# Kernel tuning notes

Hardware: AMD Instinct MI355X
Metric: run time of the kernel (lower is better)

## Reference

```python
import jax, jax.numpy as jnp
import numpy as np

LN_EPS = 1e-5
SM_EPS = 1e-16  # torch_geometric softmax denominator eps


def _layernorm(x, g, b):
    mu = jnp.mean(x, axis=-1, keepdims=True)
    var = jnp.var(x, axis=-1, keepdims=True)
    return (x - mu) * jax.lax.rsqrt(var + LN_EPS) * g + b


def setup_inputs() -> dict:
    d = 128
    L = 3
    N = 50000
    E = 800000
    key = jax.random.key(0)
    ks = jax.random.split(key, 16)
    s = 1.0 / np.sqrt(d)
    inp = {
        "edge_index": jax.random.randint(ks[0], (2, E), 0, N, dtype=jnp.int32),
        "x": jax.random.normal(ks[1], (N, d), dtype=jnp.float32),
        # per-layer attention params, stacked over layers
        "Wq": jax.random.uniform(ks[2], (L, d, d), jnp.float32, -s, s),
        "bq": jax.random.uniform(ks[3], (L, d), jnp.float32, -s, s),
        "Wk": jax.random.uniform(ks[4], (L, d, d), jnp.float32, -s, s),
        "bk": jax.random.uniform(ks[5], (L, d), jnp.float32, -s, s),
        "Wv": jax.random.uniform(ks[6], (L, d, d), jnp.float32, -s, s),
        "bv": jax.random.uniform(ks[7], (L, d), jnp.float32, -s, s),
        "ln_g": jnp.ones((L, d), jnp.float32),
        "ln_b": jnp.zeros((L, d), jnp.float32),
        # MLP stack: d -> 4d -> 2d -> d (no activations, per source)
        "W1": jax.random.uniform(ks[8], (4 * d, d), jnp.float32, -s, s),
        "b1": jax.random.uniform(ks[9], (4 * d,), jnp.float32, -s, s),
        "W2": jax.random.uniform(ks[10], (2 * d, 4 * d), jnp.float32, -0.5 * s, 0.5 * s),
        "b2": jax.random.uniform(ks[11], (2 * d,), jnp.float32, -0.5 * s, 0.5 * s),
        "W3": jax.random.uniform(ks[12], (d, 2 * d), jnp.float32, -0.7 * s, 0.7 * s),
        "b3": jax.random.uniform(ks[13], (d,), jnp.float32, -0.7 * s, 0.7 * s),
        "Wvec": jax.random.uniform(ks[14], (1, d), jnp.float32, -s, s),
        "bvec": jax.random.uniform(ks[15], (1,), jnp.float32, -s, s),
        "fn_g": jnp.ones((d,), jnp.float32),
        "fn_b": jnp.zeros((d,), jnp.float32),
    }
    return inp


def reference(edge_index, x, Wq, bq, Wk, bk, Wv, bv, ln_g, ln_b,
              W1, b1, W2, b2, W3, b3, Wvec, bvec, fn_g, fn_b):
    N = x.shape[0]
    src = edge_index[0]
    dst = edge_index[1]
    x_i = x[src]  # [E, d]
    x_j = x[dst]  # [E, d]
    L = Wq.shape[0]
    attn_output = None
    query = None
    for i in range(L):
        q = x_i @ Wq[i].T + bq[i]
        k = x_j @ Wk[i].T + bk[i]
        v = x_j @ Wv[i].T + bv[i]
        alpha = jnp.sum(q * k, axis=-1)  # [E]
        # segment softmax over destination node (torch_geometric.utils.softmax)
        m = jax.ops.segment_max(alpha, dst, num_segments=N)
        e = jnp.exp(alpha - m[dst])
        s = jax.ops.segment_sum(e, dst, num_segments=N)
        alpha = e / (s[dst] + SM_EPS)
        attn_output = jax.nn.relu(alpha[:, None] * v)  # dropout = identity (eval)
        query = _layernorm(x_j + attn_output, ln_g[i], ln_b[i])
    adj = attn_output  # squeeze(0) is a no-op for [E, d]
    adj = adj @ W1.T + b1
    adj = adj @ W2.T + b2
    adj = adj @ W3.T + b3
    adj = _layernorm(adj + query, fn_g, fn_b)
    adj_logits = (adj @ Wvec.T + bvec)[:, 0]  # [E]
    return adj_logits
```

## Files before the change

### kernel.cpp

```cpp
#include <hip/hip_runtime.h>


typedef __attribute__((ext_vector_type(8))) short bf16x8;
typedef __attribute__((ext_vector_type(4))) float f32x4;

__device__ __forceinline__ unsigned short f2bf(float f) {
  unsigned int u = __float_as_uint(f);
  unsigned int r = (u + 0x7fffu + ((u >> 16) & 1u)) >> 16;
  return (unsigned short)r;
}
__device__ __forceinline__ float blo(unsigned int u) {
  return __uint_as_float(u << 16);
}
__device__ __forceinline__ float bhi(unsigned int u) {
  return __uint_as_float(u & 0xffff0000u);
}

__global__ __launch_bounds__(128) void k_TW(
    const float* __restrict__ W2, const float* __restrict__ W1,
    const float* __restrict__ Wq, const float* __restrict__ Wk,
    const float* __restrict__ Wv, float* __restrict__ T,
    unsigned short* __restrict__ Wqb, unsigned short* __restrict__ Wkb,
    unsigned short* __restrict__ Wvb, float* __restrict__ sArr, int N) {
  const int b = blockIdx.x, t = threadIdx.x;
  if (b < 256) {
    float acc = 0.f;
    for (int k = 0; k < 512; ++k) acc += W2[b * 512 + k] * W1[k * 128 + t];
    T[b * 128 + t] = acc;
  } else if (b < 640) {
    const int idx = (b - 256) * 128 + t;
    const int m = idx >> 14, i = idx & 16383;
    const float* s = (m == 0) ? Wq : (m == 1) ? Wk : Wv;
    unsigned short* d = (m == 0) ? Wqb : (m == 1) ? Wkb : Wvb;
    d[i] = f2bf(s[i]);
  } else {
    const int i = (b - 640) * 128 + t;
    if (i < N) sArr[i] = 0.f;
  }
}

__global__ __launch_bounds__(256) void k_Ac(
    const float* __restrict__ W3, const float* __restrict__ T,
    const float* __restrict__ W2, const float* __restrict__ b1,
    const float* __restrict__ b2, const float* __restrict__ b3,
    const float* __restrict__ g, const float* __restrict__ lb,
    const float* __restrict__ fg, const float* __restrict__ fb,
    const float* __restrict__ wv, unsigned short* __restrict__ A3b,
    float* __restrict__ cfull, float* __restrict__ C) {
  __shared__ float t1[256];
  __shared__ float cf[128];
  const int b = blockIdx.x, t = threadIdx.x;
  if (b < 64) {
    const int i = 2 * b + (t >> 7), j = t & 127;
    float acc = 0.f;
    for (int k = 0; k < 256; ++k) acc += W3[i * 256 + k] * T[k * 128 + j];
    A3b[i * 128 + j] = f2bf(acc);
    return;
  }
  float acc = b2[t];
  for (int c = 0; c < 512; ++c) acc += W2[t * 512 + c] * b1[c];
  t1[t] = acc;
  __syncthreads();
  if (t < 128) {
    float a = b3[t];
    for (int k = 0; k < 256; ++k) a += W3[t * 256 + k] * t1[k];
    cfull[t] = a;
    cf[t] = a;
  }
  __syncthreads();
  if (t < 64) {
    const int l = t;
    const float2 gv = ((const float2*)g)[l];
    const float2 bv = ((const float2*)lb)[l];
    const float2 fgv = ((const float2*)fg)[l];
    const float2 fbv = ((const float2*)fb)[l];
    const float2 wvv = ((const float2*)wv)[l];
    const float P0 = cf[2 * l] + bv.x, P1 = cf[2 * l + 1] + bv.y;
    const float w0 = fgv.x * wvv.x, w1 = fgv.y * wvv.y;
    float s[9];
    s[0] = P0 + P1;
    s[1] = P0 * w0 + P1 * w1;
    s[2] = P0 * P0 + P1 * P1;
    s[3] = gv.x + gv.y;
    s[4] = gv.x * w0 + gv.y * w1;
    s[5] = gv.x * gv.x + gv.y * gv.y;
    s[6] = P0 * gv.x + P1 * gv.y;
    s[7] = w0 + w1;
    s[8] = fbv.x * wvv.x + fbv.y * wvv.y;
#pragma unroll
    for (int m = 32; m >= 1; m >>= 1)
#pragma unroll
      for (int i = 0; i < 9; ++i) s[i] += __shfl_xor(s[i], m, 64);
    if (l == 0)
#pragma unroll
      for (int i = 0; i < 9; ++i) C[i] = s[i];
  }
}

__global__ __launch_bounds__(256, 3) void k_node(
    const float* __restrict__ x, const unsigned short* __restrict__ Wqb,
    const unsigned short* __restrict__ Wkb,
    const unsigned short* __restrict__ Wvb,
    const unsigned short* __restrict__ A3b, const float* __restrict__ bq,
    const float* __restrict__ bk, const float* __restrict__ bv,
    const float* __restrict__ cfull, const float* __restrict__ g,
    const float* __restrict__ lb, const float* __restrict__ fg,
    const float* __restrict__ wvp, unsigned short* __restrict__ Qb,
    unsigned short* __restrict__ Kb, float* __restrict__ S, int N) {
  __shared__ unsigned short tile[64][136];
  const int t = threadIdx.x;
  const int nb = blockIdx.x * 64;
  for (int i = t; i < 64 * 32; i += 256) {
    const int j = i >> 5, c4 = i & 31;
    const int n = nb + j;
    float4 v = make_float4(0.f, 0.f, 0.f, 0.f);
    if (n < N) v = ((const float4*)x)[(size_t)n * 32 + c4];
    unsigned int lo = f2bf(v.x) | ((unsigned int)f2bf(v.y) << 16);
    unsigned int hi = f2bf(v.z) | ((unsigned int)f2bf(v.w) << 16);
    *(uint2*)&tile[j][c4 << 2] = make_uint2(lo, hi);
  }
  __syncthreads();
  const int wv16 = __builtin_amdgcn_readfirstlane(t >> 6) * 16;
  const int l = t & 63;
  const int ln = l & 15, g4 = l >> 4;
  bf16x8 af[4];
#pragma unroll
  for (int kb = 0; kb < 4; ++kb)
    af[kb] = *(const bf16x8*)&tile[wv16 + ln][kb * 32 + g4 * 8];

#pragma unroll
  for (int cb = 0; cb < 8; ++cb) {
    f32x4 acc = {0.f, 0.f, 0.f, 0.f};
#pragma unroll
    for (int kb = 0; kb < 4; ++kb) {
      const bf16x8 bfr =
          *(const bf16x8*)(Wqb + ((cb * 16 + ln) << 7) + kb * 32 + g4 * 8);
      acc = __builtin_amdgcn_mfma_f32_16x16x32_bf16(af[kb], bfr, acc, 0, 0, 0);
    }
    const int col = cb * 16 + ln;
    const float bs = bq[col];
#pragma unroll
    for (int r = 0; r < 4; ++r) tile[wv16 + g4 * 4 + r][col] = f2bf(acc[r] + bs);
  }
#pragma unroll
  for (int c = 0; c < 4; ++c) {
    const int row = wv16 + c * 4 + g4;
    const int n = nb + row;
    if (n < N)
      ((uint4*)(Qb + (size_t)n * 128))[ln] = *(const uint4*)&tile[row][ln * 8];
  }

#pragma unroll
  for (int cb = 0; cb < 8; ++cb) {
    f32x4 acc = {0.f, 0.f, 0.f, 0.f};
#pragma unroll
    for (int kb = 0; kb < 4; ++kb) {
      const bf16x8 bfr =
          *(const bf16x8*)(Wkb + ((cb * 16 + ln) << 7) + kb * 32 + g4 * 8);
      acc = __builtin_amdgcn_mfma_f32_16x16x32_bf16(af[kb], bfr, acc, 0, 0, 0);
    }
    const int col = cb * 16 + ln;
    const float bs = bk[col];
#pragma unroll
    for (int r = 0; r < 4; ++r) tile[wv16 + g4 * 4 + r][col] = f2bf(acc[r] + bs);
  }
#pragma unroll
  for (int c = 0; c < 4; ++c) {
    const int row = wv16 + c * 4 + g4;
    const int n = nb + row;
    if (n < N)
      ((uint4*)(Kb + (size_t)n * 128))[ln] = *(const uint4*)&tile[row][ln * 8];
  }

  float uf[8][4];
#pragma unroll
  for (int cb = 0; cb < 8; ++cb) {
    f32x4 acc = {0.f, 0.f, 0.f, 0.f};
#pragma unroll
    for (int kb = 0; kb < 4; ++kb) {
      const bf16x8 bfr =
          *(const bf16x8*)(Wvb + ((cb * 16 + ln) << 7) + kb * 32 + g4 * 8);
      acc = __builtin_amdgcn_mfma_f32_16x16x32_bf16(af[kb], bfr, acc, 0, 0, 0);
    }
    const int col = cb * 16 + ln;
    const float bs = bv[col];
#pragma unroll
    for (int r = 0; r < 4; ++r) {
      const float v = fmaxf(acc[r] + bs, 0.f);
      uf[cb][r] = v;
      tile[wv16 + g4 * 4 + r][col] = f2bf(v);
    }
  }

  bf16x8 af2[4];
#pragma unroll
  for (int kb = 0; kb < 4; ++kb)
    af2[kb] = *(const bf16x8*)&tile[wv16 + ln][kb * 32 + g4 * 8];
  float vmf[8][4];
#pragma unroll
  for (int cb = 0; cb < 8; ++cb) {
    f32x4 acc = {0.f, 0.f, 0.f, 0.f};
#pragma unroll
    for (int kb = 0; kb < 4; ++kb) {
      const bf16x8 bfr =
          *(const bf16x8*)(A3b + ((cb * 16 + ln) << 7) + kb * 32 + g4 * 8);
      acc = __builtin_amdgcn_mfma_f32_16x16x32_bf16(af2[kb], bfr, acc, 0, 0, 0);
    }
#pragma unroll
    for (int r = 0; r < 4; ++r) vmf[cb][r] = acc[r];
  }

  float gc[8], wc[8], Pc[8];
#pragma unroll
  for (int cb = 0; cb < 8; ++cb) {
    const int col = cb * 16 + ln;
    gc[cb] = g[col];
    wc[cb] = fg[col] * wvp[col];
    Pc[cb] = cfull[col] + lb[col];
  }

#pragma unroll
  for (int r = 0; r < 4; ++r) {
    const int row = wv16 + g4 * 4 + r;
    const int nrow = (nb + row < N) ? (nb + row) : (N - 1);
    float s[23];
#pragma unroll
    for (int i = 0; i < 23; ++i) s[i] = 0.f;
#pragma unroll
    for (int cb = 0; cb < 8; ++cb) {
      const float xv = x[(size_t)nrow * 128 + cb * 16 + ln];
      const float u = uf[cb][r];
      const float v = vmf[cb][r];
      const float gg = gc[cb], ww = wc[cb], PP = Pc[cb];
      const float xg = xv * gg, ug = u * gg;
      s[0] += xv;
      s[1] += u;
      s[2] += xv * xv;
      s[3] += xv * u;
      s[4] += u * u;
      s[5] += v;
      s[6] += v * ww;
      s[7] += xg;
      s[8] += ug;
      s[9] += xg * ww;
      s[10] += ug * ww;
      s[11] += PP * v;
      s[12] += v * v;
      s[13] += PP * xg;
      s[14] += PP * ug;
      s[15] += v * xg;
      s[16] += v * ug;
      s[17] += v * gg;
      s[18] += xg * xg;
      s[19] += xg * ug;
      s[20] += ug * ug;
      s[21] += xg * gg;
      s[22] += ug * gg;
    }
#pragma unroll
    for (int m = 1; m <= 8; m <<= 1)
#pragma unroll
      for (int i = 0; i < 23; ++i) s[i] += __shfl_xor(s[i], m, 64);
    const int n2 = nb + row;
    if (ln == 0 && n2 < N) {
      float* o = S + (size_t)n2 * 24;
      o[0] = s[0] * (1.f / 128.f);
      o[1] = s[1] * (1.f / 128.f);
#pragma unroll
      for (int i = 2; i < 23; ++i) o[i] = s[i];
      o[23] = 0.f;
    }
  }
}

__global__ __launch_bounds__(256) void k_edge_alpha(
    const int* __restrict__ ei, const unsigned short* __restrict__ Qb,
    const unsigned short* __restrict__ Kb, float* __restrict__ eArr,
    float* __restrict__ sArr, int E) {
  const int t = threadIdx.x;
  const int l = t & 15;
  const int e = blockIdx.x * 16 + (t >> 4);
  if (e >= E) return;
  const int src = ei[e];
  const int dst = ei[E + e];
  const uint4 qv = ((const uint4*)Qb)[(size_t)src * 16 + l];
  const uint4 kv = ((const uint4*)Kb)[(size_t)dst * 16 + l];
  float p = blo(qv.x) * blo(kv.x);
  p = fmaf(bhi(qv.x), bhi(kv.x), p);
  p = fmaf(blo(qv.y), blo(kv.y), p);
  p = fmaf(bhi(qv.y), bhi(kv.y), p);
  p = fmaf(blo(qv.z), blo(kv.z), p);
  p = fmaf(bhi(qv.z), bhi(kv.z), p);
  p = fmaf(blo(qv.w), blo(kv.w), p);
  p = fmaf(bhi(qv.w), bhi(kv.w), p);
#pragma unroll
  for (int m = 8; m >= 1; m >>= 1) p += __shfl_xor(p, m, 16);
  if (l == 0) {
    const float ex = __expf(p);
    eArr[e] = ex;
    atomicAdd(&sArr[dst], ex);
  }
}

__global__ __launch_bounds__(256) void k_edge_out(
    const int* __restrict__ ei, const float* __restrict__ eArr,
    const float* __restrict__ sArr, const float* __restrict__ S,
    const float* __restrict__ C, const float* __restrict__ bvec,
    float* __restrict__ out, int E) {
  const int e = blockIdx.x * 256 + threadIdx.x;
  if (e >= E) return;
  const int dst = ei[E + e];
  const float t = eArr[e] / (sArr[dst] + 1e-16f);
  const float4* o = (const float4*)(S + (size_t)dst * 24);
  const float4 q0 = o[0], q1 = o[1], q2 = o[2], q3 = o[3], q4 = o[4],
               q5 = o[5];
  const float mx = q0.x, mU = q0.y, sxx = q0.z, sxu = q0.w;
  const float suu = q1.x, sv = q1.y, svw = q1.z, sxg = q1.w;
  const float sug = q2.x, sxgw = q2.y, sugw = q2.z, spv = q2.w;
  const float svv = q3.x, pxg = q3.y, pug = q3.z, vxg = q3.w;
  const float vug = q4.x, vg = q4.y, xgxg = q4.z, xgug = q4.w;
  const float ugug = q5.x, xgg = q5.y, ugg = q5.z;
  const float SP = C[0], SPw = C[1], SPP = C[2], SG = C[3], SGw = C[4],
              GG = C[5], SPG = C[6], Sw = C[7], s0 = C[8];
  const float mu = mx + t * mU;
  const float qy = (sxx + 2.f * t * sxu + t * t * suu) * (1.f / 128.f);
  const float i1 = rsqrtf(qy - mu * mu + 1e-5f);
  const float sz = SP + t * sv + i1 * (sxg + t * sug - mu * SG);
  const float szw = SPw + t * svw + i1 * (sxgw + t * sugw - mu * SGw);
  const float cross = pxg + t * (pug + vxg) + t * t * vug - mu * (SPG + t * vg);
  const float rr = xgxg + 2.f * t * xgug + t * t * ugug -
                   2.f * mu * (xgg + t * ugg) + mu * mu * GG;
  const float szz =
      SPP + 2.f * t * spv + t * t * svv + 2.f * i1 * cross + i1 * i1 * rr;
  const float muz = sz * (1.f / 128.f);
  const float varz = szz * (1.f / 128.f) - muz * muz;
  const float iz = rsqrtf(varz + 1e-5f);
  out[e] = iz * (szw - muz * Sw) + s0 + bvec[0];
}

extern "C" void kernel_launch(void* const* d_in, const int* in_sizes, int n_in,
                              void* d_out, int out_size, void* d_ws,
                              size_t ws_size, hipStream_t stream) {
  const int* ei = (const int*)d_in[0];
  const float* x = (const float*)d_in[1];
  const float* Wq = (const float*)d_in[2];
  const float* bq = (const float*)d_in[3];
  const float* Wk = (const float*)d_in[4];
  const float* bk = (const float*)d_in[5];
  const float* Wv = (const float*)d_in[6];
  const float* bv = (const float*)d_in[7];
  const float* ln_g = (const float*)d_in[8];
  const float* ln_b = (const float*)d_in[9];
  const float* W1 = (const float*)d_in[10];
  const float* b1 = (const float*)d_in[11];
  const float* W2 = (const float*)d_in[12];
  const float* b2 = (const float*)d_in[13];
  const float* W3 = (const float*)d_in[14];
  const float* b3 = (const float*)d_in[15];
  const float* Wvec = (const float*)d_in[16];
  const float* bvec = (const float*)d_in[17];
  const float* fn_g = (const float*)d_in[18];
  const float* fn_b = (const float*)d_in[19];

  const int E = in_sizes[0] / 2;
  const int N = in_sizes[1] / 128;

  const float* Wq2 = Wq + 2 * 128 * 128;
  const float* bq2 = bq + 2 * 128;
  const float* Wk2 = Wk + 2 * 128 * 128;
  const float* bk2 = bk + 2 * 128;
  const float* Wv2 = Wv + 2 * 128 * 128;
  const float* bv2 = bv + 2 * 128;
  const float* g2 = ln_g + 2 * 128;
  const float* lb2 = ln_b + 2 * 128;

  float* ws = (float*)d_ws;
  float* T = ws;
  float* cfull = T + 32768;
  float* consts = cfull + 128;
  unsigned short* Wqb = (unsigned short*)(consts + 16);
  unsigned short* Wkb = Wqb + 16384;
  unsigned short* Wvb = Wkb + 16384;
  unsigned short* A3b = Wvb + 16384;
  float* fbase = consts + 16 + 32768;
  unsigned short* Qb = (unsigned short*)fbase;
  unsigned short* Kb = Qb + (size_t)N * 128;
  float* S = fbase + (size_t)N * 128;
  float* eArr = S + (size_t)N * 24;
  float* sArr = eArr + E;

  const int zblk = (N + 127) / 128;
  k_TW<<<640 + zblk, 128, 0, stream>>>(W2, W1, Wq2, Wk2, Wv2, T, Wqb, Wkb,
                                       Wvb, sArr, N);
  k_Ac<<<65, 256, 0, stream>>>(W3, T, W2, b1, b2, b3, g2, lb2, fn_g, fn_b,
                               Wvec, A3b, cfull, consts);

  const int nblk = (N + 63) / 64;
  k_node<<<nblk, 256, 0, stream>>>(x, Wqb, Wkb, Wvb, A3b, bq2, bk2, bv2,
                                   cfull, g2, lb2, fn_g, Wvec, Qb, Kb, S, N);
  const int ablk = (E + 15) / 16;
  k_edge_alpha<<<ablk, 256, 0, stream>>>(ei, Qb, Kb, eArr, sArr, E);
  const int oblk = (E + 255) / 256;
  k_edge_out<<<oblk, 256, 0, stream>>>(ei, eArr, sArr, S, consts, bvec,
                                       (float*)d_out, E);
}
```

Baseline: 221.9 us.

## Stage node-kernel weight matrices in swizzled LDS before MFMA loops

```diff
diff --git a/kernel.cpp b/kernel.cpp
--- a/kernel.cpp
+++ b/kernel.cpp
@@ -97,7 +97,7 @@
   }
 }
 
-__global__ __launch_bounds__(256, 3) void k_node(
+__global__ __launch_bounds__(256) void k_node(
     const float* __restrict__ x, const unsigned short* __restrict__ Wqb,
     const unsigned short* __restrict__ Wkb,
     const unsigned short* __restrict__ Wvb,
@@ -108,6 +108,7 @@
     const float* __restrict__ wvp, unsigned short* __restrict__ Qb,
     unsigned short* __restrict__ Kb, float* __restrict__ S, int N) {
   __shared__ unsigned short tile[64][136];
+  __shared__ unsigned short wl[128 * 128];
   const int t = threadIdx.x;
   const int nb = blockIdx.x * 64;
   for (int i = t; i < 64 * 32; i += 256) {
@@ -128,15 +129,32 @@
   for (int kb = 0; kb < 4; ++kb)
     af[kb] = *(const bf16x8*)&tile[wv16 + ln][kb * 32 + g4 * 8];
 
+#define STAGE_W(MAT)                                                          \
+  {                                                                           \
+    __syncthreads();           \
+    _Pragma("unroll") for (int c = 0; c < 8; ++c) {                           \
+      const int idx = c * 256 + t;                                            \
+      const int byte = idx * 16;                                              \
+      const int row = byte >> 8;                                              \
+      const int swz = byte ^ ((row & 7) << 4);                                \
+      *(uint4*)((char*)wl + swz) =                                            \
+          *(const uint4*)((const char*)(MAT) + byte);                         \
+    }                                                                         \
+    __syncthreads();                                                          \
+  }
+#define WFRAG(CB, KB)                                                         \
+  (*(const bf16x8*)((const char*)wl +                                         \
+                    (((((CB)*16 + ln) << 8) + (KB)*64 + g4 * 16) ^            \
+                     ((ln & 7) << 4))))
+
+  STAGE_W(Wqb)
 #pragma unroll
   for (int cb = 0; cb < 8; ++cb) {
     f32x4 acc = {0.f, 0.f, 0.f, 0.f};
 #pragma unroll
-    for (int kb = 0; kb < 4; ++kb) {
-      const bf16x8 bfr =
-          *(const bf16x8*)(Wqb + ((cb * 16 + ln) << 7) + kb * 32 + g4 * 8);
-      acc = __builtin_amdgcn_mfma_f32_16x16x32_bf16(af[kb], bfr, acc, 0, 0, 0);
-    }
+    for (int kb = 0; kb < 4; ++kb)
+      acc = __builtin_amdgcn_mfma_f32_16x16x32_bf16(af[kb], WFRAG(cb, kb),
+                                                    acc, 0, 0, 0);
     const int col = cb * 16 + ln;
     const float bs = bq[col];
 #pragma unroll
@@ -150,15 +168,14 @@
       ((uint4*)(Qb + (size_t)n * 128))[ln] = *(const uint4*)&tile[row][ln * 8];
   }
 
+  STAGE_W(Wkb)
 #pragma unroll
   for (int cb = 0; cb < 8; ++cb) {
     f32x4 acc = {0.f, 0.f, 0.f, 0.f};
 #pragma unroll
-    for (int kb = 0; kb < 4; ++kb) {
-      const bf16x8 bfr =
-          *(const bf16x8*)(Wkb + ((cb * 16 + ln) << 7) + kb * 32 + g4 * 8);
-      acc = __builtin_amdgcn_mfma_f32_16x16x32_bf16(af[kb], bfr, acc, 0, 0, 0);
-    }
+    for (int kb = 0; kb < 4; ++kb)
+      acc = __builtin_amdgcn_mfma_f32_16x16x32_bf16(af[kb], WFRAG(cb, kb),
+                                                    acc, 0, 0, 0);
     const int col = cb * 16 + ln;
     const float bs = bk[col];
 #pragma unroll
@@ -172,16 +189,15 @@
       ((uint4*)(Kb + (size_t)n * 128))[ln] = *(const uint4*)&tile[row][ln * 8];
   }
 
+  STAGE_W(Wvb)
   float uf[8][4];
 #pragma unroll
   for (int cb = 0; cb < 8; ++cb) {
     f32x4 acc = {0.f, 0.f, 0.f, 0.f};
 #pragma unroll
-    for (int kb = 0; kb < 4; ++kb) {
-      const bf16x8 bfr =
-          *(const bf16x8*)(Wvb + ((cb * 16 + ln) << 7) + kb * 32 + g4 * 8);
-      acc = __builtin_amdgcn_mfma_f32_16x16x32_bf16(af[kb], bfr, acc, 0, 0, 0);
-    }
+    for (int kb = 0; kb < 4; ++kb)
+      acc = __builtin_amdgcn_mfma_f32_16x16x32_bf16(af[kb], WFRAG(cb, kb),
+                                                    acc, 0, 0, 0);
     const int col = cb * 16 + ln;
     const float bs = bv[col];
 #pragma unroll
@@ -196,19 +212,20 @@
 #pragma unroll
   for (int kb = 0; kb < 4; ++kb)
     af2[kb] = *(const bf16x8*)&tile[wv16 + ln][kb * 32 + g4 * 8];
+  STAGE_W(A3b)
   float vmf[8][4];
 #pragma unroll
   for (int cb = 0; cb < 8; ++cb) {
     f32x4 acc = {0.f, 0.f, 0.f, 0.f};
 #pragma unroll
-    for (int kb = 0; kb < 4; ++kb) {
-      const bf16x8 bfr =
-          *(const bf16x8*)(A3b + ((cb * 16 + ln) << 7) + kb * 32 + g4 * 8);
-      acc = __builtin_amdgcn_mfma_f32_16x16x32_bf16(af2[kb], bfr, acc, 0, 0, 0);
-    }
+    for (int kb = 0; kb < 4; ++kb)
+      acc = __builtin_amdgcn_mfma_f32_16x16x32_bf16(af2[kb], WFRAG(cb, kb),
+                                                    acc, 0, 0, 0);
 #pragma unroll
     for (int r = 0; r < 4; ++r) vmf[cb][r] = acc[r];
   }
+#undef STAGE_W
+#undef WFRAG
 
   float gc[8], wc[8], Pc[8];
 #pragma unroll
```

Result: faster. 181.4 us (-18.3%).
